# Kernel optimization log

Measured on AMD Instinct MI355X. Metric: run time of the kernel, lower is better.

The kernel has to match this reference:

```python
import jax, jax.numpy as jnp
import numpy as np

ZETA = 1.1
GAMMA = -0.1

B, F, D = 1024, 32, 128


def setup_inputs() -> dict:
    key = jax.random.key(0)
    k1, k2 = jax.random.split(key)
    feature = jax.random.normal(k1, (B, F, D), dtype=jnp.float32)
    # nn.Parameter init: normal(mean=0, std=0.001)
    matrix = jax.random.normal(k2, (F, F, D, D), dtype=jnp.float32) * 0.001
    return {"feature": feature, "matrix": matrix}


def reference(feature, matrix):
    # feature: [B, F, D]; matrix (logAlpha of hard-concrete gate): [F, F, D, D]
    nF = matrix.shape[0]
    # strict upper-triangular pair mask over (i, j)
    mask = jnp.triu(jnp.ones((nF, nF), dtype=feature.dtype), k=1)
    # deterministic (eval-mode) hard-concrete gate: stretch + clamp
    s = jax.nn.sigmoid(matrix)
    z = jnp.clip(s * (ZETA - GAMMA) + GAMMA, 0.0, 1.0)
    l0_out = mask[:, :, None, None] * z  # [F, F, D, D]
    # out[b,i,j] = f_i^T Z_ij f_j  == sum_{d,e} f[b,i,d] * Z[i,j,d,e] * f[b,j,e]
    # (faithful to: (f[:, :, None, :, None] @ f[:, None, :, None, :]) * Z, summed over (d, e))
    out = jnp.einsum('bid,ijde,bje->bij', feature, l0_out, feature)
    return out
```

## Files before the change

### kernel.cpp

```cpp
#include <hip/hip_runtime.h>

#define F_SZ 32
#define D_SZ 128
#define FD   4096
#define NPAIR 496
#define LDZ  136

typedef __bf16 bf16x8 __attribute__((ext_vector_type(8)));
typedef float floatx4 __attribute__((ext_vector_type(4)));

__device__ __forceinline__ unsigned short f2bf(float f) {
  unsigned u = __float_as_uint(f);
  u += 0x7fffu + ((u >> 16) & 1u);
  return (unsigned short)(u >> 16);
}
__device__ __forceinline__ float bf2f(unsigned short h) {
  return __uint_as_float(((unsigned)h) << 16);
}
__device__ __forceinline__ void decode_pair(int p, int& io, int& jo) {
  int i = 0;
  while (p >= F_SZ - 1 - i) { p -= F_SZ - 1 - i; ++i; }
  io = i; jo = i + 1 + p;
}

__global__ __launch_bounds__(256)
void prep(const float* __restrict__ mat, const float* __restrict__ feat,
          unsigned short* __restrict__ Zt, unsigned short* __restrict__ fb) {
  const int t = threadIdx.x;
  if (blockIdx.x < NPAIR) {
    __shared__ unsigned short tile[128 * LDZ];
    int i, j; decode_pair(blockIdx.x, i, j);
    const float* zp = mat + (((size_t)i * F_SZ + j) << 14);
    #pragma unroll 8
    for (int it = 0; it < 64; ++it) {
      int idx = it * 256 + t;
      int d = idx >> 7, e = idx & 127;
      float v = zp[idx];
      float s = 1.0f / (1.0f + __expf(-v));
      float z = fminf(1.0f, fmaxf(0.0f, fmaf(s, 1.2f, -0.1f)));
      tile[e * LDZ + d] = f2bf(z);
    }
    __syncthreads();
    unsigned short* op = Zt + ((size_t)blockIdx.x << 14);
    #pragma unroll 4
    for (int it = 0; it < 16; ++it) {
      int idx4 = it * 256 + t;
      int e = idx4 >> 5, d4 = idx4 & 31;
      *(ushort4*)&op[idx4 * 4] = *(const ushort4*)&tile[e * LDZ + d4 * 4];
    }
  } else {
    const int blk = blockIdx.x - NPAIR;
    #pragma unroll 4
    for (int k = 0; k < 16; ++k) {
      size_t v4 = (size_t)blk * 4096 + k * 256 + t;
      float4 v = ((const float4*)feat)[v4];
      ushort4 h;
      h.x = f2bf(v.x); h.y = f2bf(v.y); h.z = f2bf(v.z); h.w = f2bf(v.w);
      *(ushort4*)(fb + v4 * 4) = h;
    }
  }
}

__global__ __launch_bounds__(256, 3)
void pair_gemm(const unsigned short* __restrict__ Zt,
               const unsigned short* __restrict__ fb,
               float* __restrict__ out) {
  __shared__ unsigned short sZ[128 * LDZ];
  int i, j; decode_pair(blockIdx.x, i, j);
  const int t = threadIdx.x;
  const int lane = t & 63, l15 = lane & 15, quad = lane >> 4;
  const int w = t >> 6;
  const int rowbase = blockIdx.y * 128 + w * 32;

  {
    const unsigned short* zp = Zt + ((size_t)blockIdx.x << 14);
    #pragma unroll
    for (int r = 0; r < 8; ++r) {
      int s = r * 256 + t;
      int row = s >> 4, c = s & 15;
      uint4 v = *(const uint4*)(zp + s * 8);
      *(uint4*)&sZ[row * LDZ + c * 8] = v;
    }
  }

  floatx4 acc[8][2];
  #pragma unroll
  for (int mf = 0; mf < 8; ++mf) {
    acc[mf][0] = (floatx4){0.f, 0.f, 0.f, 0.f};
    acc[mf][1] = (floatx4){0.f, 0.f, 0.f, 0.f};
  }
  __syncthreads();

  const unsigned short* fbp0 = fb + (size_t)(rowbase + l15) * FD + i * D_SZ + quad * 8;
  const unsigned short* fbp1 = fbp0 + 16 * FD;
  #pragma unroll
  for (int ks = 0; ks < 4; ++ks) {
    bf16x8 B0 = *(const bf16x8*)(fbp0 + ks * 32);
    bf16x8 B1 = *(const bf16x8*)(fbp1 + ks * 32);
    #pragma unroll
    for (int mf = 0; mf < 8; ++mf) {
      bf16x8 A = *(const bf16x8*)&sZ[(mf * 16 + l15) * LDZ + ks * 32 + quad * 8];
      acc[mf][0] = __builtin_amdgcn_mfma_f32_16x16x32_bf16(A, B0, acc[mf][0], 0, 0, 0);
      acc[mf][1] = __builtin_amdgcn_mfma_f32_16x16x32_bf16(A, B1, acc[mf][1], 0, 0, 0);
    }
  }

  #pragma unroll
  for (int nf = 0; nf < 2; ++nf) {
    const int b = rowbase + nf * 16 + l15;
    const unsigned short* fjp = fb + (size_t)b * FD + j * D_SZ + quad * 4;
    float pl = 0.f;
    #pragma unroll
    for (int mf = 0; mf < 8; ++mf) {
      ushort4 fh = *(const ushort4*)(fjp + mf * 16);
      floatx4 c = acc[mf][nf];
      pl = fmaf(c[0], bf2f(fh.x), pl);
      pl = fmaf(c[1], bf2f(fh.y), pl);
      pl = fmaf(c[2], bf2f(fh.z), pl);
      pl = fmaf(c[3], bf2f(fh.w), pl);
    }
    pl += __shfl_xor(pl, 16, 64);
    pl += __shfl_xor(pl, 32, 64);
    if (quad == 0)
      out[(size_t)b * (F_SZ * F_SZ) + i * F_SZ + j] = pl;
  }
}

#define LDA  136
#define LDB  136
__global__ __launch_bounds__(256, 2)
void interaction_pair_kernel(const float* __restrict__ feat,
                             const float* __restrict__ mat,
                             float* __restrict__ out) {
  __shared__ unsigned short sA[128 * LDA];
  __shared__ unsigned short sBT[128 * LDB];
  const int t = threadIdx.x;
  const int w = t >> 6, lane = t & 63, l15 = lane & 15, quad = lane >> 4;
  int i, j; decode_pair(blockIdx.x, i, j);
  {
    const float* zp = mat + (((size_t)i * F_SZ + j) << 14);
    #pragma unroll 8
    for (int it = 0; it < 64; ++it) {
      int idx = it * 256 + t;
      int d = idx >> 7, e = idx & 127;
      float v = zp[idx];
      float s = 1.0f / (1.0f + __expf(-v));
      float z = fminf(1.0f, fmaxf(0.0f, fmaf(s, 1.2f, -0.1f)));
      sBT[e * LDB + d] = f2bf(z);
    }
  }
  for (int bt = 0; bt < 8; ++bt) {
    const int b0 = bt * 128;
    #pragma unroll 4
    for (int it = 0; it < 16; ++it) {
      int idx4 = it * 256 + t;
      int r = idx4 >> 5, c4 = idx4 & 31;
      const float4 v = *(const float4*)(feat + (size_t)(b0 + r) * FD + i * D_SZ + c4 * 4);
      ushort4 h;
      h.x = f2bf(v.x); h.y = f2bf(v.y); h.z = f2bf(v.z); h.w = f2bf(v.w);
      *(ushort4*)(&sA[r * LDA + c4 * 4]) = h;
    }
    __syncthreads();
    floatx4 acc[2][8];
    #pragma unroll
    for (int mf = 0; mf < 2; ++mf)
      #pragma unroll
      for (int nf = 0; nf < 8; ++nf)
        acc[mf][nf] = (floatx4){0.f, 0.f, 0.f, 0.f};
    #pragma unroll
    for (int k0 = 0; k0 < 128; k0 += 32) {
      const int kc = k0 + quad * 8;
      bf16x8 a0 = *(const bf16x8*)&sA[(w * 32 +      l15) * LDA + kc];
      bf16x8 a1 = *(const bf16x8*)&sA[(w * 32 + 16 + l15) * LDA + kc];
      #pragma unroll
      for (int nf = 0; nf < 8; ++nf) {
        bf16x8 bfr = *(const bf16x8*)&sBT[(nf * 16 + l15) * LDB + kc];
        acc[0][nf] = __builtin_amdgcn_mfma_f32_16x16x32_bf16(a0, bfr, acc[0][nf], 0, 0, 0);
        acc[1][nf] = __builtin_amdgcn_mfma_f32_16x16x32_bf16(a1, bfr, acc[1][nf], 0, 0, 0);
      }
    }
    #pragma unroll
    for (int mf = 0; mf < 2; ++mf) {
      float pl[4] = {0.f, 0.f, 0.f, 0.f};
      const int rb = w * 32 + mf * 16 + quad * 4;
      #pragma unroll
      for (int nf = 0; nf < 8; ++nf) {
        const int col = nf * 16 + l15;
        const float* fj = feat + (size_t)(b0 + rb) * FD + j * D_SZ + col;
        floatx4 c = acc[mf][nf];
        pl[0] += c[0] * fj[0];
        pl[1] += c[1] * fj[FD];
        pl[2] += c[2] * fj[2 * FD];
        pl[3] += c[3] * fj[3 * FD];
      }
      #pragma unroll
      for (int off = 1; off < 16; off <<= 1) {
        pl[0] += __shfl_xor(pl[0], off, 64);
        pl[1] += __shfl_xor(pl[1], off, 64);
        pl[2] += __shfl_xor(pl[2], off, 64);
        pl[3] += __shfl_xor(pl[3], off, 64);
      }
      if (l15 == 0) {
        size_t ob = (size_t)(b0 + rb) * (F_SZ * F_SZ) + (size_t)i * F_SZ + j;
        out[ob]                   = pl[0];
        out[ob + 1 * F_SZ * F_SZ] = pl[1];
        out[ob + 2 * F_SZ * F_SZ] = pl[2];
        out[ob + 3 * F_SZ * F_SZ] = pl[3];
      }
    }
    __syncthreads();
  }
}

extern "C" void kernel_launch(void* const* d_in, const int* in_sizes, int n_in,
                              void* d_out, int out_size, void* d_ws, size_t ws_size,
                              hipStream_t stream) {
  const float* feat = (const float*)d_in[0];
  const float* mat  = (const float*)d_in[1];
  float* out = (float*)d_out;

  hipMemsetAsync(out, 0, (size_t)out_size * sizeof(float), stream);

  const size_t zt_bytes = (size_t)NPAIR * D_SZ * D_SZ * sizeof(unsigned short);
  const size_t fb_bytes = (size_t)1024 * FD * sizeof(unsigned short);

  if (ws_size >= zt_bytes + fb_bytes) {
    unsigned short* Zt = (unsigned short*)d_ws;
    unsigned short* fbuf = Zt + (size_t)NPAIR * D_SZ * D_SZ;
    prep<<<dim3(NPAIR + 256), dim3(256), 0, stream>>>(mat, feat, Zt, fbuf);
    pair_gemm<<<dim3(NPAIR, 8), dim3(256), 0, stream>>>(Zt, fbuf, out);
  } else {
    interaction_pair_kernel<<<dim3(NPAIR), dim3(256), 0, stream>>>(feat, mat, out);
  }
}
```

Baseline: 160.9 us.

## Fuse Z gate computation into pair GEMM and register-cache Z fragments

Removes the separate Zt workspace: each pair block now reads the fp32 logAlpha matrix, applies sigmoid+clamp, and writes the transposed bf16 tile into shared memory directly. It also preloads all Z fragments into registers and loops over four batch tiles per block (grid y shrinks from 8 to 2), with occupancy bounds lowered to 2. This avoids a round trip of a large bf16 intermediate through global memory. In exchange, the gate math is repeated by each of the two y-blocks, and register pressure rises.

```diff
diff --git a/kernel.cpp b/kernel.cpp
--- a/kernel.cpp
+++ b/kernel.cpp
@@ -24,12 +24,30 @@
 }
 
 __global__ __launch_bounds__(256)
-void prep(const float* __restrict__ mat, const float* __restrict__ feat,
-          unsigned short* __restrict__ Zt, unsigned short* __restrict__ fb) {
+void prep_f(const float* __restrict__ feat, unsigned short* __restrict__ fb) {
   const int t = threadIdx.x;
-  if (blockIdx.x < NPAIR) {
-    __shared__ unsigned short tile[128 * LDZ];
-    int i, j; decode_pair(blockIdx.x, i, j);
+  const int blk = blockIdx.x;
+  #pragma unroll 4
+  for (int k = 0; k < 16; ++k) {
+    size_t v4 = (size_t)blk * 4096 + k * 256 + t;
+    float4 v = ((const float4*)feat)[v4];
+    ushort4 h;
+    h.x = f2bf(v.x); h.y = f2bf(v.y); h.z = f2bf(v.z); h.w = f2bf(v.w);
+    *(ushort4*)(fb + v4 * 4) = h;
+  }
+}
+
+__global__ __launch_bounds__(256, 2)
+void pair_gemm(const float* __restrict__ mat,
+               const unsigned short* __restrict__ fb,
+               float* __restrict__ out) {
+  __shared__ unsigned short sZ[128 * LDZ];
+  int i, j; decode_pair(blockIdx.x, i, j);
+  const int t = threadIdx.x;
+  const int lane = t & 63, l15 = lane & 15, quad = lane >> 4;
+  const int w = t >> 6;
+
+  {
     const float* zp = mat + (((size_t)i * F_SZ + j) << 14);
     #pragma unroll 8
     for (int it = 0; it < 64; ++it) {
@@ -38,91 +56,66 @@
       float v = zp[idx];
       float s = 1.0f / (1.0f + __expf(-v));
       float z = fminf(1.0f, fmaxf(0.0f, fmaf(s, 1.2f, -0.1f)));
-      tile[e * LDZ + d] = f2bf(z);
-    }
-    __syncthreads();
-    unsigned short* op = Zt + ((size_t)blockIdx.x << 14);
-    #pragma unroll 4
-    for (int it = 0; it < 16; ++it) {
-      int idx4 = it * 256 + t;
-      int e = idx4 >> 5, d4 = idx4 & 31;
-      *(ushort4*)&op[idx4 * 4] = *(const ushort4*)&tile[e * LDZ + d4 * 4];
-    }
-  } else {
-    const int blk = blockIdx.x - NPAIR;
-    #pragma unroll 4
-    for (int k = 0; k < 16; ++k) {
-      size_t v4 = (size_t)blk * 4096 + k * 256 + t;
-      float4 v = ((const float4*)feat)[v4];
-      ushort4 h;
-      h.x = f2bf(v.x); h.y = f2bf(v.y); h.z = f2bf(v.z); h.w = f2bf(v.w);
-      *(ushort4*)(fb + v4 * 4) = h;
-    }
-  }
-}
-
-__global__ __launch_bounds__(256, 3)
-void pair_gemm(const unsigned short* __restrict__ Zt,
-               const unsigned short* __restrict__ fb,
-               float* __restrict__ out) {
-  __shared__ unsigned short sZ[128 * LDZ];
-  int i, j; decode_pair(blockIdx.x, i, j);
-  const int t = threadIdx.x;
-  const int lane = t & 63, l15 = lane & 15, quad = lane >> 4;
-  const int w = t >> 6;
-  const int rowbase = blockIdx.y * 128 + w * 32;
-
-  {
-    const unsigned short* zp = Zt + ((size_t)blockIdx.x << 14);
-    #pragma unroll
-    for (int r = 0; r < 8; ++r) {
-      int s = r * 256 + t;
-      int row = s >> 4, c = s & 15;
-      uint4 v = *(const uint4*)(zp + s * 8);
-      *(uint4*)&sZ[row * LDZ + c * 8] = v;
-    }
-  }
-
-  floatx4 acc[8][2];
+      sZ[e * LDZ + d] = f2bf(z);
+    }
+  }
+  __syncthreads();
+
+  bf16x8 A[8][4];
   #pragma unroll
-  for (int mf = 0; mf < 8; ++mf) {
-    acc[mf][0] = (floatx4){0.f, 0.f, 0.f, 0.f};
-    acc[mf][1] = (floatx4){0.f, 0.f, 0.f, 0.f};
-  }
-  __syncthreads();
-
-  const unsigned short* fbp0 = fb + (size_t)(rowbase + l15) * FD + i * D_SZ + quad * 8;
-  const unsigned short* fbp1 = fbp0 + 16 * FD;
-  #pragma unroll
-  for (int ks = 0; ks < 4; ++ks) {
-    bf16x8 B0 = *(const bf16x8*)(fbp0 + ks * 32);
-    bf16x8 B1 = *(const bf16x8*)(fbp1 + ks * 32);
+  for (int mf = 0; mf < 8; ++mf)
+    #pragma unroll
+    for (int ks = 0; ks < 4; ++ks)
+      A[mf][ks] = *(const bf16x8*)&sZ[(mf * 16 + l15) * LDZ + ks * 32 + quad * 8];
+
+  const int bhalf = blockIdx.y * 512;
+
+  #pragma unroll 2
+  for (int itb = 0; itb < 4; ++itb) {
+    const int rowbase = bhalf + itb * 128 + w * 32;
+
+    const unsigned short* fbp0 = fb + (size_t)(rowbase + l15) * FD + i * D_SZ + quad * 8;
+    bf16x8 B0[4], B1[4];
+    #pragma unroll
+    for (int ks = 0; ks < 4; ++ks) {
+      B0[ks] = *(const bf16x8*)(fbp0 + ks * 32);
+      B1[ks] = *(const bf16x8*)(fbp0 + 16 * FD + ks * 32);
+    }
+
+    floatx4 acc[8][2];
     #pragma unroll
     for (int mf = 0; mf < 8; ++mf) {
-      bf16x8 A = *(const bf16x8*)&sZ[(mf * 16 + l15) * LDZ + ks * 32 + quad * 8];
-      acc[mf][0] = __builtin_amdgcn_mfma_f32_16x16x32_bf16(A, B0, acc[mf][0], 0, 0, 0);
-      acc[mf][1] = __builtin_amdgcn_mfma_f32_16x16x32_bf16(A, B1, acc[mf][1], 0, 0, 0);
-    }
-  }
-
-  #pragma unroll
-  for (int nf = 0; nf < 2; ++nf) {
-    const int b = rowbase + nf * 16 + l15;
-    const unsigned short* fjp = fb + (size_t)b * FD + j * D_SZ + quad * 4;
-    float pl = 0.f;
-    #pragma unroll
-    for (int mf = 0; mf < 8; ++mf) {
-      ushort4 fh = *(const ushort4*)(fjp + mf * 16);
-      floatx4 c = acc[mf][nf];
-      pl = fmaf(c[0], bf2f(fh.x), pl);
-      pl = fmaf(c[1], bf2f(fh.y), pl);
-      pl = fmaf(c[2], bf2f(fh.z), pl);
-      pl = fmaf(c[3], bf2f(fh.w), pl);
-    }
-    pl += __shfl_xor(pl, 16, 64);
-    pl += __shfl_xor(pl, 32, 64);
-    if (quad == 0)
-      out[(size_t)b * (F_SZ * F_SZ) + i * F_SZ + j] = pl;
+      acc[mf][0] = (floatx4){0.f, 0.f, 0.f, 0.f};
+      acc[mf][1] = (floatx4){0.f, 0.f, 0.f, 0.f};
+    }
+
+    #pragma unroll
+    for (int ks = 0; ks < 4; ++ks)
+      #pragma unroll
+      for (int mf = 0; mf < 8; ++mf) {
+        acc[mf][0] = __builtin_amdgcn_mfma_f32_16x16x32_bf16(A[mf][ks], B0[ks], acc[mf][0], 0, 0, 0);
+        acc[mf][1] = __builtin_amdgcn_mfma_f32_16x16x32_bf16(A[mf][ks], B1[ks], acc[mf][1], 0, 0, 0);
+      }
+
+    #pragma unroll
+    for (int nf = 0; nf < 2; ++nf) {
+      const int b = rowbase + nf * 16 + l15;
+      const unsigned short* fjp = fb + (size_t)b * FD + j * D_SZ + quad * 4;
+      float pl = 0.f;
+      #pragma unroll
+      for (int mf = 0; mf < 8; ++mf) {
+        ushort4 fh = *(const ushort4*)(fjp + mf * 16);
+        floatx4 c = acc[mf][nf];
+        pl = fmaf(c[0], bf2f(fh.x), pl);
+        pl = fmaf(c[1], bf2f(fh.y), pl);
+        pl = fmaf(c[2], bf2f(fh.z), pl);
+        pl = fmaf(c[3], bf2f(fh.w), pl);
+      }
+      pl += __shfl_xor(pl, 16, 64);
+      pl += __shfl_xor(pl, 32, 64);
+      if (quad == 0)
+        out[(size_t)b * (F_SZ * F_SZ) + i * F_SZ + j] = pl;
+    }
   }
 }
 
@@ -221,14 +214,12 @@
 
   hipMemsetAsync(out, 0, (size_t)out_size * sizeof(float), stream);
 
-  const size_t zt_bytes = (size_t)NPAIR * D_SZ * D_SZ * sizeof(unsigned short);
   const size_t fb_bytes = (size_t)1024 * FD * sizeof(unsigned short);
 
-  if (ws_size >= zt_bytes + fb_bytes) {
-    unsigned short* Zt = (unsigned short*)d_ws;
-    unsigned short* fbuf = Zt + (size_t)NPAIR * D_SZ * D_SZ;
-    prep<<<dim3(NPAIR + 256), dim3(256), 0, stream>>>(mat, feat, Zt, fbuf);
-    pair_gemm<<<dim3(NPAIR, 8), dim3(256), 0, stream>>>(Zt, fbuf, out);
+  if (ws_size >= fb_bytes) {
+    unsigned short* fbuf = (unsigned short*)d_ws;
+    prep_f<<<dim3(256), dim3(256), 0, stream>>>(feat, fbuf);
+    pair_gemm<<<dim3(NPAIR, 2), dim3(256), 0, stream>>>(mat, fbuf, out);
   } else {
     interaction_pair_kernel<<<dim3(NPAIR), dim3(256), 0, stream>>>(feat, mat, out);
   }
```

Measured after the change: 158.0 us. Within noise of the previous version (-1.8%).

## Transpose bf16 features to field-major layout and double batch rows per GEMM block

Applied to the files above, without the earlier changes.

The prep kernel now writes the bf16 copy of the features in [F][B][D] layout, so each pair_gemm block reads contiguous 256-byte rows for fields i and j instead of rows strided by 8 KB. The Z transpose in prep is split into two half-tiles per pair, which doubles the prep grid and halves its shared memory. pair_gemm now covers 256 batch rows per block in two passes over the same shared-memory Z tile, preloads the B fragments into registers, and raises launch_bounds occupancy to 4. Together these aim to cut global-memory stride overhead and the number of times Z is loaded into LDS, at the cost of an uncoalesced gather when prep transposes the features.

```diff
diff --git a/kernel.cpp b/kernel.cpp
--- a/kernel.cpp
+++ b/kernel.cpp
@@ -5,6 +5,7 @@
 #define FD   4096
 #define NPAIR 496
 #define LDZ  136
+#define LDH  68
 
 typedef __bf16 bf16x8 __attribute__((ext_vector_type(8)));
 typedef float floatx4 __attribute__((ext_vector_type(4)));
@@ -25,52 +26,54 @@
 
 __global__ __launch_bounds__(256)
 void prep(const float* __restrict__ mat, const float* __restrict__ feat,
-          unsigned short* __restrict__ Zt, unsigned short* __restrict__ fb) {
+          unsigned short* __restrict__ Zt, unsigned short* __restrict__ fbI) {
   const int t = threadIdx.x;
-  if (blockIdx.x < NPAIR) {
-    __shared__ unsigned short tile[128 * LDZ];
-    int i, j; decode_pair(blockIdx.x, i, j);
-    const float* zp = mat + (((size_t)i * F_SZ + j) << 14);
+  if (blockIdx.x < 2 * NPAIR) {
+    __shared__ unsigned short tile[128 * LDH];
+    const int pair = blockIdx.x >> 1;
+    const int yh = blockIdx.x & 1;
+    int i, j; decode_pair(pair, i, j);
+    const float* zp = mat + (((size_t)i * F_SZ + j) << 14) + (size_t)yh * 64 * 128;
     #pragma unroll 8
-    for (int it = 0; it < 64; ++it) {
+    for (int it = 0; it < 32; ++it) {
       int idx = it * 256 + t;
-      int d = idx >> 7, e = idx & 127;
+      int dd = idx >> 7, e = idx & 127;
       float v = zp[idx];
       float s = 1.0f / (1.0f + __expf(-v));
       float z = fminf(1.0f, fmaxf(0.0f, fmaf(s, 1.2f, -0.1f)));
-      tile[e * LDZ + d] = f2bf(z);
+      tile[e * LDH + dd] = f2bf(z);
     }
     __syncthreads();
-    unsigned short* op = Zt + ((size_t)blockIdx.x << 14);
-    #pragma unroll 4
-    for (int it = 0; it < 16; ++it) {
+    unsigned short* op = Zt + ((size_t)pair << 14) + yh * 64;
+    #pragma unroll
+    for (int it = 0; it < 8; ++it) {
       int idx4 = it * 256 + t;
-      int e = idx4 >> 5, d4 = idx4 & 31;
-      *(ushort4*)&op[idx4 * 4] = *(const ushort4*)&tile[e * LDZ + d4 * 4];
+      int e = idx4 >> 4, d4 = idx4 & 15;
+      *(ushort4*)&op[e * 128 + d4 * 4] = *(const ushort4*)&tile[e * LDH + d4 * 4];
     }
   } else {
-    const int blk = blockIdx.x - NPAIR;
-    #pragma unroll 4
-    for (int k = 0; k < 16; ++k) {
-      size_t v4 = (size_t)blk * 4096 + k * 256 + t;
-      float4 v = ((const float4*)feat)[v4];
+    const int blk = blockIdx.x - 2 * NPAIR;
+    #pragma unroll
+    for (int it = 0; it < 8; ++it) {
+      size_t g = (size_t)blk * 2048 + it * 256 + t;
+      int f = (int)(g >> 15), b = (int)((g >> 5) & 1023), d4 = (int)(g & 31);
+      float4 v = ((const float4*)feat)[(size_t)b * 1024 + f * 32 + d4];
       ushort4 h;
       h.x = f2bf(v.x); h.y = f2bf(v.y); h.z = f2bf(v.z); h.w = f2bf(v.w);
-      *(ushort4*)(fb + v4 * 4) = h;
-    }
-  }
-}
-
-__global__ __launch_bounds__(256, 3)
+      *(ushort4*)(fbI + g * 4) = h;
+    }
+  }
+}
+
+__global__ __launch_bounds__(256, 4)
 void pair_gemm(const unsigned short* __restrict__ Zt,
-               const unsigned short* __restrict__ fb,
+               const unsigned short* __restrict__ fbI,
                float* __restrict__ out) {
   __shared__ unsigned short sZ[128 * LDZ];
   int i, j; decode_pair(blockIdx.x, i, j);
   const int t = threadIdx.x;
   const int lane = t & 63, l15 = lane & 15, quad = lane >> 4;
   const int w = t >> 6;
-  const int rowbase = blockIdx.y * 128 + w * 32;
 
   {
     const unsigned short* zp = Zt + ((size_t)blockIdx.x << 14);
@@ -82,47 +85,58 @@
       *(uint4*)&sZ[row * LDZ + c * 8] = v;
     }
   }
-
-  floatx4 acc[8][2];
-  #pragma unroll
-  for (int mf = 0; mf < 8; ++mf) {
-    acc[mf][0] = (floatx4){0.f, 0.f, 0.f, 0.f};
-    acc[mf][1] = (floatx4){0.f, 0.f, 0.f, 0.f};
-  }
   __syncthreads();
 
-  const unsigned short* fbp0 = fb + (size_t)(rowbase + l15) * FD + i * D_SZ + quad * 8;
-  const unsigned short* fbp1 = fbp0 + 16 * FD;
-  #pragma unroll
-  for (int ks = 0; ks < 4; ++ks) {
-    bf16x8 B0 = *(const bf16x8*)(fbp0 + ks * 32);
-    bf16x8 B1 = *(const bf16x8*)(fbp1 + ks * 32);
+  const unsigned short* fbi = fbI + ((size_t)i << 17);
+  const unsigned short* fbj = fbI + ((size_t)j << 17);
+
+  #pragma unroll 1
+  for (int itb = 0; itb < 2; ++itb) {
+    const int rowbase = blockIdx.y * 256 + itb * 128 + w * 32;
+
+    const unsigned short* fbp0 = fbi + (size_t)(rowbase + l15) * D_SZ + quad * 8;
+    bf16x8 B0[4], B1[4];
+    #pragma unroll
+    for (int ks = 0; ks < 4; ++ks) {
+      B0[ks] = *(const bf16x8*)(fbp0 + ks * 32);
+      B1[ks] = *(const bf16x8*)(fbp0 + 16 * D_SZ + ks * 32);
+    }
+
+    floatx4 acc[8][2];
     #pragma unroll
     for (int mf = 0; mf < 8; ++mf) {
-      bf16x8 A = *(const bf16x8*)&sZ[(mf * 16 + l15) * LDZ + ks * 32 + quad * 8];
-      acc[mf][0] = __builtin_amdgcn_mfma_f32_16x16x32_bf16(A, B0, acc[mf][0], 0, 0, 0);
-      acc[mf][1] = __builtin_amdgcn_mfma_f32_16x16x32_bf16(A, B1, acc[mf][1], 0, 0, 0);
-    }
-  }
-
-  #pragma unroll
-  for (int nf = 0; nf < 2; ++nf) {
-    const int b = rowbase + nf * 16 + l15;
-    const unsigned short* fjp = fb + (size_t)b * FD + j * D_SZ + quad * 4;
-    float pl = 0.f;
-    #pragma unroll
-    for (int mf = 0; mf < 8; ++mf) {
-      ushort4 fh = *(const ushort4*)(fjp + mf * 16);
-      floatx4 c = acc[mf][nf];
-      pl = fmaf(c[0], bf2f(fh.x), pl);
-      pl = fmaf(c[1], bf2f(fh.y), pl);
-      pl = fmaf(c[2], bf2f(fh.z), pl);
-      pl = fmaf(c[3], bf2f(fh.w), pl);
-    }
-    pl += __shfl_xor(pl, 16, 64);
-    pl += __shfl_xor(pl, 32, 64);
-    if (quad == 0)
-      out[(size_t)b * (F_SZ * F_SZ) + i * F_SZ + j] = pl;
+      acc[mf][0] = (floatx4){0.f, 0.f, 0.f, 0.f};
+      acc[mf][1] = (floatx4){0.f, 0.f, 0.f, 0.f};
+    }
+
+    #pragma unroll
+    for (int ks = 0; ks < 4; ++ks)
+      #pragma unroll
+      for (int mf = 0; mf < 8; ++mf) {
+        bf16x8 A = *(const bf16x8*)&sZ[(mf * 16 + l15) * LDZ + ks * 32 + quad * 8];
+        acc[mf][0] = __builtin_amdgcn_mfma_f32_16x16x32_bf16(A, B0[ks], acc[mf][0], 0, 0, 0);
+        acc[mf][1] = __builtin_amdgcn_mfma_f32_16x16x32_bf16(A, B1[ks], acc[mf][1], 0, 0, 0);
+      }
+
+    #pragma unroll
+    for (int nf = 0; nf < 2; ++nf) {
+      const int b = rowbase + nf * 16 + l15;
+      const unsigned short* fjp = fbj + (size_t)b * D_SZ + quad * 4;
+      float pl = 0.f;
+      #pragma unroll
+      for (int mf = 0; mf < 8; ++mf) {
+        ushort4 fh = *(const ushort4*)(fjp + mf * 16);
+        floatx4 c = acc[mf][nf];
+        pl = fmaf(c[0], bf2f(fh.x), pl);
+        pl = fmaf(c[1], bf2f(fh.y), pl);
+        pl = fmaf(c[2], bf2f(fh.z), pl);
+        pl = fmaf(c[3], bf2f(fh.w), pl);
+      }
+      pl += __shfl_xor(pl, 16, 64);
+      pl += __shfl_xor(pl, 32, 64);
+      if (quad == 0)
+        out[(size_t)b * (F_SZ * F_SZ) + i * F_SZ + j] = pl;
+    }
   }
 }
 
@@ -225,10 +239,10 @@
   const size_t fb_bytes = (size_t)1024 * FD * sizeof(unsigned short);
 
   if (ws_size >= zt_bytes + fb_bytes) {
-    unsigned short* Zt = (unsigned short*)d_ws;
-    unsigned short* fbuf = Zt + (size_t)NPAIR * D_SZ * D_SZ;
-    prep<<<dim3(NPAIR + 256), dim3(256), 0, stream>>>(mat, feat, Zt, fbuf);
-    pair_gemm<<<dim3(NPAIR, 8), dim3(256), 0, stream>>>(Zt, fbuf, out);
+    unsigned short* Zt  = (unsigned short*)d_ws;
+    unsigned short* fbI = Zt + (size_t)NPAIR * D_SZ * D_SZ;
+    prep<<<dim3(2 * NPAIR + 512), dim3(256), 0, stream>>>(mat, feat, Zt, fbI);
+    pair_gemm<<<dim3(NPAIR, 4), dim3(256), 0, stream>>>(Zt, fbI, out);
   } else {
     interaction_pair_kernel<<<dim3(NPAIR), dim3(256), 0, stream>>>(feat, mat, out);
   }
```

Result: slower. 266.0 us (+65.3%).
